# Kernel tuning notes

Hardware: AMD Instinct MI355X
Metric: run time of the kernel (lower is better)

Reference implementation:

```python
import jax, jax.numpy as jnp
import numpy as np

H = 256          # lstm_size
VOCAB = 6        # num_branches + 1
NBR = 5          # num_branches
TEMP = 5.0
OP_TANH = 1.1 / 2.5
BLOCKS, SEQ = 16, 2048


def setup_inputs() -> dict:
    key = jax.random.key(0)
    ks = jax.random.split(key, 12)
    def gw(k, shape, scale=0.05):
        return jax.random.normal(k, shape, dtype=jnp.float32) * scale
    return {
        "arc": jax.random.randint(ks[0], (BLOCKS, SEQ), 0, VOCAB, dtype=jnp.int32),
        "h0": gw(ks[1], (2, 1, H), 0.01),
        "c0": gw(ks[2], (2, 1, H), 0.01),
        "emb": gw(ks[3], (VOCAB, H)),
        "Wih_f": gw(ks[4], (4 * H, H)), "Whh_f": gw(ks[5], (4 * H, H)),
        "bih_f": jnp.zeros(4 * H, jnp.float32), "bhh_f": jnp.zeros(4 * H, jnp.float32),
        "Wih_b": gw(ks[6], (4 * H, H)), "Whh_b": gw(ks[7], (4 * H, H)),
        "bih_b": jnp.zeros(4 * H, jnp.float32), "bhh_b": jnp.zeros(4 * H, jnp.float32),
        "fcW": gw(ks[8], (NBR, 2 * H)), "fcb": jnp.zeros(NBR, jnp.float32),
    }


def _lstm_dir(x, h0, c0, Wih, Whh, bih, bhh):
    # x: [T,H]; one direction of a 1-layer LSTM, PyTorch gate order (i,f,g,o)
    def step(carry, xt):
        h, c = carry
        g = xt @ Wih.T + h @ Whh.T + bih + bhh          # [4H]
        i, f, gg, o = jnp.split(g, 4)
        i, f, o = jax.nn.sigmoid(i), jax.nn.sigmoid(f), jax.nn.sigmoid(o)
        c = f * c + i * jnp.tanh(gg)
        h = o * jnp.tanh(c)
        return (h, c), h
    (hT, cT), hs = jax.lax.scan(step, (h0, c0), x)
    return hs, hT, cT


def reference(arc, h0, c0, emb, Wih_f, Whh_f, bih_f, bhh_f,
              Wih_b, Whh_b, bih_b, bhh_b, fcW, fcb):
    key0 = jax.random.key(42)

    def block(carry, arc_i):
        hf, cf, hb, cb, key = carry
        key, sub = jax.random.split(key)
        x = emb[arc_i]                                   # [T,H]
        hs_f, hfT, cfT = _lstm_dir(x, hf, cf, Wih_f, Whh_f, bih_f, bhh_f)
        hs_b, hbT, cbT = _lstm_dir(x[::-1], hb, cb, Wih_b, Whh_b, bih_b, bhh_b)
        out = jnp.concatenate([hs_f, hs_b[::-1]], axis=-1)   # [T,2H]
        logits = (out @ fcW.T + fcb) / TEMP
        logits = OP_TANH * jnp.tanh(logits)              # [T,5]
        logp = jax.nn.log_softmax(logits, axis=-1)
        prob = jnp.exp(logp)
        idx = jax.random.categorical(sub, logits, axis=-1)   # multinomial(softmax(logits))
        # F.cross_entropy(logits, idx) == mean NLL of sampled indices
        ce = -jnp.mean(jnp.take_along_axis(logp, idx[:, None], axis=-1))
        # original: -mean(sum(logp*prob over size-1 dim)) == -mean over [T,5]
        ent = jax.lax.stop_gradient(-jnp.mean(logp * prob))
        return (hfT, cfT, hbT, cbT, key), (idx, ce, ent)

    init = (h0[0, 0], c0[0, 0], h0[1, 0], c0[1, 0], key0)
    (hfT, cfT, hbT, cbT, _), (all_arc, ces, ents) = jax.lax.scan(block, init, arc)
    h = jnp.stack([hfT, hbT])[:, None, :]                # [2,1,H]
    c = jnp.stack([cfT, cbT])[:, None, :]
    return all_arc, jnp.sum(ces), jnp.sum(ents), h, c
```

## Files before the change

kernel.cpp:

```cpp
#include <hip/hip_runtime.h>
#include <math.h>
#include <stdint.h>

static constexpr int XG_OFF   = 0;
static constexpr int MBA_OFF  = 12288;
static constexpr int MBB_OFF  = 14336;
static constexpr int ELEC_OFF = 16384;
static constexpr int SH_OFF   = 20480;
static constexpr int SC_OFF   = 20992;
static constexpr int HIST_OFF = 21504;
static constexpr int HIST_D   = 524288;
static constexpr int CEP_OFF  = 1070080;
static constexpr int ENTP_OFF = 1070144;

static constexpr int OUT_CE = 32768;
static constexpr int OUT_H  = 32770;
static constexpr int OUT_C  = 33282;

__device__ __forceinline__ void st_sc0(unsigned long long* p, unsigned long long v) {
  asm volatile("global_store_dwordx2 %0, %1, off sc0" :: "v"(p), "v"(v) : "memory");
}
__device__ __forceinline__ unsigned long long ld_sc0(const unsigned long long* p) {
  unsigned long long r;
  asm volatile("global_load_dwordx2 %0, %1, off sc0\n\ts_waitcnt vmcnt(0)"
               : "=&v"(r) : "v"(p) : "memory");
  return r;
}

__device__ __forceinline__ uint32_t rotl32(uint32_t v, int n) {
  return (v << n) | (v >> (32 - n));
}
__device__ __forceinline__ void tf2x32(uint32_t k0, uint32_t k1,
                                       uint32_t x0, uint32_t x1,
                                       uint32_t& y0, uint32_t& y1) {
  const uint32_t k2 = k0 ^ k1 ^ 0x1BD11BDAu;
  x0 += k0; x1 += k1;
  x0 += x1; x1 = rotl32(x1, 13); x1 ^= x0;
  x0 += x1; x1 = rotl32(x1, 15); x1 ^= x0;
  x0 += x1; x1 = rotl32(x1, 26); x1 ^= x0;
  x0 += x1; x1 = rotl32(x1, 6);  x1 ^= x0;
  x0 += k1; x1 += k2 + 1u;
  x0 += x1; x1 = rotl32(x1, 17); x1 ^= x0;
  x0 += x1; x1 = rotl32(x1, 29); x1 ^= x0;
  x0 += x1; x1 = rotl32(x1, 16); x1 ^= x0;
  x0 += x1; x1 = rotl32(x1, 24); x1 ^= x0;
  x0 += k2; x1 += k0 + 2u;
  x0 += x1; x1 = rotl32(x1, 13); x1 ^= x0;
  x0 += x1; x1 = rotl32(x1, 15); x1 ^= x0;
  x0 += x1; x1 = rotl32(x1, 26); x1 ^= x0;
  x0 += x1; x1 = rotl32(x1, 6);  x1 ^= x0;
  x0 += k0; x1 += k1 + 3u;
  x0 += x1; x1 = rotl32(x1, 17); x1 ^= x0;
  x0 += x1; x1 = rotl32(x1, 29); x1 ^= x0;
  x0 += x1; x1 = rotl32(x1, 16); x1 ^= x0;
  x0 += x1; x1 = rotl32(x1, 24); x1 ^= x0;
  x0 += k1; x1 += k2 + 4u;
  x0 += x1; x1 = rotl32(x1, 13); x1 ^= x0;
  x0 += x1; x1 = rotl32(x1, 15); x1 ^= x0;
  x0 += x1; x1 = rotl32(x1, 26); x1 ^= x0;
  x0 += x1; x1 = rotl32(x1, 6);  x1 ^= x0;
  x0 += k2; x1 += k0 + 5u;
  y0 = x0; y1 = x1;
}

__device__ __forceinline__ float gumbel_from_bits(uint32_t bits) {
  float f = __uint_as_float(0x3f800000u | (bits >> 9)) - 1.0f;
  const float tiny = __uint_as_float(0x00800000u);
  float u = fmaxf(tiny, f + tiny);
  float l1 = (float)log((double)u);
  return -(float)log(-(double)l1);
}

__global__ void k_xg(const float* __restrict__ emb,
                     const float* __restrict__ WihF, const float* __restrict__ bihF,
                     const float* __restrict__ bhhF,
                     const float* __restrict__ WihB, const float* __restrict__ bihB,
                     const float* __restrict__ bhhB,
                     float* __restrict__ ws) {
  __shared__ float se[1536];
  const int tid = threadIdx.x;
  for (int i = tid; i < 1536; i += 256) se[i] = emb[i];
  __syncthreads();
  const int gid = blockIdx.x * 256 + tid;
  const int d = gid >> 10, r = gid & 1023;
  const float* Wih = d ? WihB : WihF;
  const float* bih = d ? bihB : bihF;
  const float* bhh = d ? bhhB : bhhF;
  float acc[6] = {0.f, 0.f, 0.f, 0.f, 0.f, 0.f};
  const float4* wr = (const float4*)(Wih + r * 256);
  for (int c = 0; c < 64; c++) {
    float4 wv = wr[c];
#pragma unroll
    for (int v = 0; v < 6; v++) {
      const float* ev = &se[v * 256 + 4 * c];
      acc[v] += wv.x * ev[0] + wv.y * ev[1] + wv.z * ev[2] + wv.w * ev[3];
    }
  }
  const float bsum = bih[r] + bhh[r];
#pragma unroll
  for (int v = 0; v < 6; v++) ws[XG_OFF + d * 6144 + v * 1024 + r] = acc[v] + bsum;
}

__global__ void k_zero(float* __restrict__ ws) {
  if (threadIdx.x < 16) ((int*)(ws + ELEC_OFF))[threadIdx.x] = 0;
}

__global__ __launch_bounds__(256, 1)
void k_chain(const int* __restrict__ arc, const float* __restrict__ h0,
             const float* __restrict__ c0, const float* __restrict__ WhhF,
             const float* __restrict__ WhhB, float* __restrict__ ws,
             float* __restrict__ out, int b) {
  const int tid = threadIdx.x;
  __shared__ int role_s;
  __shared__ float xg_l[768];
  __shared__ int arc_s[2048];
  __shared__ float h_s[2][320];

  if (tid == 0) {
    int xcc;
    asm volatile("s_getreg_b32 %0, hwreg(HW_REG_XCC_ID)" : "=s"(xcc));
    xcc &= 7;
    int* cnt = (int*)(ws + ELEC_OFF);
    int* winner = cnt + 8;
    int pos = __hip_atomic_fetch_add(&cnt[xcc], 1, __ATOMIC_RELAXED,
                                     __HIP_MEMORY_SCOPE_AGENT);
    if (pos == 15) {
      int expected = 0;
      __hip_atomic_compare_exchange_strong(winner, &expected, xcc + 1,
          __ATOMIC_RELAXED, __ATOMIC_RELAXED, __HIP_MEMORY_SCOPE_AGENT);
    }
    int wv;
    do {
      wv = __hip_atomic_load(winner, __ATOMIC_RELAXED, __HIP_MEMORY_SCOPE_AGENT);
    } while (wv == 0);
    role_s = (pos < 16 && wv == xcc + 1) ? pos : -1;
  }
  __syncthreads();
  const int role = role_s;
  if (role < 0) return;

  const int d = role >> 3;
  const int k = role & 7;
  const int w = tid >> 6;
  const int lane = tid & 63;
  const int q = lane >> 4, p = lane & 15;

  const float* Whh = d ? WhhB : WhhF;
  for (int i = tid; i < 768; i += 256) {
    const int sym = i >> 7, r = i & 127, el = r >> 2, g = r & 3;
    xg_l[i] = ws[XG_OFF + d * 6144 + sym * 1024 + g * 256 + 32 * k + el];
  }
  {
    const int* ab = arc + b * 2048;
    for (int i = tid; i < 2048; i += 256) arc_s[i] = ab[i];
  }
  const int eA = 32 * k + 8 * w + 2 * q;
  const int elA = 8 * w + 2 * q;
  float Wr[8][16];
#pragma unroll
  for (int i = 0; i < 8; i++) {
    const int R = 256 * (i >> 1) + eA + (i & 1);
    const float4* rp = (const float4*)(Whh + R * 256 + 16 * p);
#pragma unroll
    for (int j = 0; j < 4; j++) {
      const float4 v = rp[j];
      Wr[i][4 * j + 0] = v.x;
      Wr[i][4 * j + 1] = v.y;
      Wr[i][4 * j + 2] = v.z;
      Wr[i][4 * j + 3] = v.w;
    }
  }
#pragma unroll
  for (int i = 0; i < 8; i++)
#pragma unroll
    for (int c = 0; c < 16; c++)
      asm volatile("" : "+v"(Wr[i][c]));
  const float* hprev = (b == 0) ? (h0 + d * 256) : (ws + SH_OFF + d * 256);
  float4 hw[4];
#pragma unroll
  for (int j = 0; j < 4; j++) hw[j] = ((const float4*)(hprev + 16 * p))[j];
  float cA = (b == 0) ? c0[d * 256 + eA] : ws[SC_OFF + d * 256 + eA];
  float cB = (b == 0) ? c0[d * 256 + eA + 1] : ws[SC_OFF + d * 256 + eA + 1];
  float hA = 0.f, hB = 0.f;
  __syncthreads();

  unsigned long long* mbA = (unsigned long long*)(ws + MBA_OFF);
  unsigned long long* mbB = (unsigned long long*)(ws + MBB_OFF);
  const unsigned stampBase = (unsigned)b * 2048u;
  float* histD = ws + HIST_OFF + d * HIST_D;
  const bool selfPoll = ((tid >> 5) == k);
  int lim = 24, fails = 0;

  for (int t = 0; t < 2048; t++) {
    float acc[8];
#pragma unroll
    for (int i = 0; i < 8; i++) {
      float a;
      a  = Wr[i][0]  * hw[0].x;
      a += Wr[i][1]  * hw[0].y;
      a += Wr[i][2]  * hw[0].z;
      a += Wr[i][3]  * hw[0].w;
      a += Wr[i][4]  * hw[1].x;
      a += Wr[i][5]  * hw[1].y;
      a += Wr[i][6]  * hw[1].z;
      a += Wr[i][7]  * hw[1].w;
      a += Wr[i][8]  * hw[2].x;
      a += Wr[i][9]  * hw[2].y;
      a += Wr[i][10] * hw[2].z;
      a += Wr[i][11] * hw[2].w;
      a += Wr[i][12] * hw[3].x;
      a += Wr[i][13] * hw[3].y;
      a += Wr[i][14] * hw[3].z;
      a += Wr[i][15] * hw[3].w;
      acc[i] = a;
    }
#pragma unroll
    for (int i = 0; i < 8; i++) {
      float v = acc[i];
      v += __shfl_xor(v, 1, 16);
      v += __shfl_xor(v, 2, 16);
      v += __shfl_xor(v, 4, 16);
      v += __shfl_xor(v, 8, 16);
      acc[i] = v;
    }
    const int sym = arc_s[d ? (2047 - t) : t];
    const float4 xgA = *(const float4*)&xg_l[sym * 128 + elA * 4];
    const float4 xgB = *(const float4*)&xg_l[sym * 128 + elA * 4 + 4];
    {
      const float gi = acc[0] + xgA.x;
      const float gf = acc[2] + xgA.y;
      const float gg = acc[4] + xgA.z;
      const float go = acc[6] + xgA.w;
      const float I = 1.0f / (1.0f + expf(-gi));
      const float F = 1.0f / (1.0f + expf(-gf));
      const float G = tanhf(gg);
      const float O = 1.0f / (1.0f + expf(-go));
      cA = F * cA + I * G;
      hA = O * tanhf(cA);
    }
    {
      const float gi = acc[1] + xgB.x;
      const float gf = acc[3] + xgB.y;
      const float gg = acc[5] + xgB.z;
      const float go = acc[7] + xgB.w;
      const float I = 1.0f / (1.0f + expf(-gi));
      const float F = 1.0f / (1.0f + expf(-gf));
      const float G = tanhf(gg);
      const float O = 1.0f / (1.0f + expf(-go));
      cB = F * cB + I * G;
      hB = O * tanhf(cB);
    }
    const unsigned S = stampBase + (unsigned)t + 1u;
    const int mbo = (d * 2 + (t & 1)) * 256;
    unsigned long long* mbAp = mbA + mbo;
    unsigned long long* mbBp = mbB + mbo;
    const int np = (t + 1) & 1;
    if (p < 2) {
      const int e = eA + p;
      const float hv = p ? hB : hA;
      const unsigned long long pk = (unsigned long long)__float_as_uint(hv) |
                                    ((unsigned long long)S << 32);
      __hip_atomic_store(&mbBp[e], pk, __ATOMIC_RELAXED, __HIP_MEMORY_SCOPE_AGENT);
      st_sc0(&mbAp[e], pk);
      histD[t * 256 + e] = hv;
      h_s[np][(e >> 4) * 20 + (e & 15)] = hv;
    }
    asm volatile("s_waitcnt vmcnt(0)" ::: "memory");
    if (t == 2047) break;
    {
      unsigned long long v = 0;
      bool got = false;
      for (int it = 0; it < lim; ++it) {
        unsigned long long f = selfPoll ? 0ull : ld_sc0(&mbAp[tid]);
        bool ok = selfPoll | ((unsigned)(f >> 32) == S);
        if (__all(ok)) { v = f; got = true; break; }
      }
      if (!got) {
        if (++fails >= 4) lim = 0;
        for (;;) {
          unsigned long long f = selfPoll ? 0ull :
              __hip_atomic_load(&mbBp[tid], __ATOMIC_RELAXED,
                                __HIP_MEMORY_SCOPE_AGENT);
          bool ok = selfPoll | ((unsigned)(f >> 32) == S);
          if (__all(ok)) { v = f; break; }
        }
      }
      if (!selfPoll)
        h_s[np][(tid >> 4) * 20 + (tid & 15)] = __uint_as_float((unsigned)v);
    }
    __syncthreads();
    {
      const float4* hp = (const float4*)&h_s[np][20 * p];
#pragma unroll
      for (int j = 0; j < 4; j++) hw[j] = hp[j];
    }
  }

  if (p < 2) {
    const int e = eA + p;
    ws[SH_OFF + d * 256 + e] = p ? hB : hA;
    ws[SC_OFF + d * 256 + e] = p ? cB : cA;
    if (b == 15) {
      out[OUT_H + d * 256 + e] = p ? hB : hA;
      out[OUT_C + d * 256 + e] = p ? cB : cA;
    }
  }
}

__global__ void k_sampler(const float* __restrict__ fcW, const float* __restrict__ fcb,
                          float* __restrict__ ws, float* __restrict__ out, int b) {
  const int tid = threadIdx.x;
  __shared__ float sW[5 * 512];
  __shared__ float sb[5];
  __shared__ float red[256];
  for (int i = tid; i < 2560; i += 256) sW[i] = fcW[i];
  if (tid < 5) sb[tid] = fcb[tid];
  __syncthreads();
  uint32_t s0 = 0u, s1 = 0u;
  {
    uint32_t k0 = 0u, k1 = 42u;
    for (int i = 0; i <= b; i++) {
      uint32_t n0, n1, t0, t1;
      tf2x32(k0, k1, 0u, 0u, n0, n1);
      tf2x32(k0, k1, 0u, 1u, t0, t1);
      s0 = t0; s1 = t1;
      k0 = n0; k1 = n1;
    }
  }
  const int pp = blockIdx.x * 256 + tid;
  const float* histF = ws + HIST_OFF;
  const float* histB = ws + HIST_OFF + HIST_D;
  float dotL[5] = {0.f, 0.f, 0.f, 0.f, 0.f};
  float dotH[5] = {0.f, 0.f, 0.f, 0.f, 0.f};
  const float4* hfL = (const float4*)(histF + pp * 256);
  const float4* hbL = (const float4*)(histB + (2047 - pp) * 256);
  const float4* hfH = (const float4*)(histF + (pp + 1024) * 256);
  const float4* hbH = (const float4*)(histB + (1023 - pp) * 256);
  for (int c = 0; c < 64; c++) {
    float4 a = hfL[c], bb = hbL[c], e = hfH[c], f = hbH[c];
#pragma unroll
    for (int j = 0; j < 5; j++) {
      const float* wr = &sW[j * 512 + 4 * c];
      dotL[j] += a.x * wr[0] + a.y * wr[1] + a.z * wr[2] + a.w * wr[3];
      dotL[j] += bb.x * wr[256] + bb.y * wr[257] + bb.z * wr[258] + bb.w * wr[259];
      dotH[j] += e.x * wr[0] + e.y * wr[1] + e.z * wr[2] + e.w * wr[3];
      dotH[j] += f.x * wr[256] + f.y * wr[257] + f.z * wr[258] + f.w * wr[259];
    }
  }
  uint32_t bl[5], bh[5];
#pragma unroll
  for (int j = 0; j < 5; j++) {
    uint32_t y0, y1;
    tf2x32(s0, s1, 0u, (uint32_t)(5 * pp + j), y0, y1);
    bl[j] = y0 ^ y1;
    tf2x32(s0, s1, 0u, (uint32_t)(5 * (pp + 1024) + j), y0, y1);
    bh[j] = y0 ^ y1;
  }
  const float OPT = (float)(1.1 / 2.5);
  float ce_acc = 0.f, ent_acc = 0.f;
#pragma unroll
  for (int half = 0; half < 2; half++) {
    const int t = half ? (pp + 1024) : pp;
    float l[5];
#pragma unroll
    for (int j = 0; j < 5; j++) {
      float dv = half ? dotH[j] : dotL[j];
      l[j] = OPT * tanhf((dv + sb[j]) / 5.0f);
    }
    int idx = 0;
    float best;
    {
      uint32_t b0 = half ? bh[0] : bl[0];
      best = gumbel_from_bits(b0) + l[0];
    }
#pragma unroll
    for (int j = 1; j < 5; j++) {
      uint32_t bj = half ? bh[j] : bl[j];
      float v = gumbel_from_bits(bj) + l[j];
      if (v > best) { best = v; idx = j; }
    }
    out[b * 2048 + t] = (float)idx;
    float m = l[0];
#pragma unroll
    for (int j = 1; j < 5; j++) m = fmaxf(m, l[j]);
    float ssum = 0.f;
#pragma unroll
    for (int j = 0; j < 5; j++) ssum += expf(l[j] - m);
    float lse = logf(ssum);
    float lpidx = 0.f;
#pragma unroll
    for (int j = 0; j < 5; j++) {
      float lp = (l[j] - m) - lse;
      ent_acc -= lp * expf(lp);
      lpidx = (j == idx) ? lp : lpidx;
    }
    ce_acc -= lpidx;
  }
  red[tid] = ce_acc; __syncthreads();
  for (int s = 128; s > 0; s >>= 1) {
    if (tid < s) red[tid] += red[tid + s];
    __syncthreads();
  }
  if (tid == 0) ws[CEP_OFF + b * 4 + blockIdx.x] = red[0];
  __syncthreads();
  red[tid] = ent_acc; __syncthreads();
  for (int s = 128; s > 0; s >>= 1) {
    if (tid < s) red[tid] += red[tid + s];
    __syncthreads();
  }
  if (tid == 0) ws[ENTP_OFF + b * 4 + blockIdx.x] = red[0];
}

__global__ void k_final(const float* __restrict__ ws, float* __restrict__ out) {
  if (threadIdx.x == 0 && blockIdx.x == 0) {
    float ce = 0.f, ent = 0.f;
    for (int b = 0; b < 16; b++) {
      float cb = 0.f, eb = 0.f;
      for (int j = 0; j < 4; j++) {
        cb += ws[CEP_OFF + b * 4 + j];
        eb += ws[ENTP_OFF + b * 4 + j];
      }
      ce += cb / 2048.0f;
      ent += eb / 10240.0f;
    }
    out[OUT_CE] = ce;
    out[OUT_CE + 1] = ent;
  }
}

extern "C" void kernel_launch(void* const* d_in, const int* in_sizes, int n_in,
                              void* d_out, int out_size, void* d_ws, size_t ws_size,
                              hipStream_t stream) {
  (void)in_sizes; (void)n_in; (void)out_size; (void)ws_size;
  const int* arc = (const int*)d_in[0];
  const float* h0 = (const float*)d_in[1];
  const float* c0 = (const float*)d_in[2];
  const float* emb = (const float*)d_in[3];
  const float* WihF = (const float*)d_in[4];
  const float* WhhF = (const float*)d_in[5];
  const float* bihF = (const float*)d_in[6];
  const float* bhhF = (const float*)d_in[7];
  const float* WihB = (const float*)d_in[8];
  const float* WhhB = (const float*)d_in[9];
  const float* bihB = (const float*)d_in[10];
  const float* bhhB = (const float*)d_in[11];
  const float* fcW = (const float*)d_in[12];
  const float* fcb = (const float*)d_in[13];
  float* out = (float*)d_out;
  float* ws = (float*)d_ws;

  hipLaunchKernelGGL(k_xg, dim3(8), dim3(256), 0, stream,
                     emb, WihF, bihF, bhhF, WihB, bihB, bhhB, ws);
  for (int b = 0; b < 16; b++) {
    hipLaunchKernelGGL(k_zero, dim3(1), dim3(64), 0, stream, ws);
    hipLaunchKernelGGL(k_chain, dim3(128), dim3(256), 0, stream,
                       arc, h0, c0, WhhF, WhhB, ws, out, b);
    hipLaunchKernelGGL(k_sampler, dim3(4), dim3(256), 0, stream,
                       fcW, fcb, ws, out, b);
  }
  hipLaunchKernelGGL(k_final, dim3(1), dim3(64), 0, stream, ws, out);
}
```

Before: 63.25 ms.

## Spread mailbox polling across non-producer lanes and keep losing blocks spinning

Each non-producer lane now polls one remote mailbox entry with per-lane retry loops, replacing the wave-wide __all polling over 256 entries with self-skip. The vmcnt(0) wait after stores is removed, and the full __syncthreads becomes lgkmcnt wait plus a raw s_barrier. Blocks that lose the election no longer exit. They spin on FMA work until role 0 sets a done flag, apparently to keep clocks or occupancy steady. The risks are memory-ordering hazards from dropping the vmcnt wait, and wasted power from the spinning blocks.

Result: slower. 68.72 ms (+8.6%).

```diff
diff --git a/kernel.cpp b/kernel.cpp
--- a/kernel.cpp
+++ b/kernel.cpp
@@ -137,7 +137,18 @@
   }
   __syncthreads();
   const int role = role_s;
-  if (role < 0) return;
+  if (role < 0) {
+    int* done = (int*)(ws + ELEC_OFF) + 9;
+    float x = (float)tid + 1.5f;
+    for (;;) {
+#pragma unroll
+      for (int i = 0; i < 512; i++) x = __builtin_fmaf(x, 1.0000001f, 1e-7f);
+      asm volatile("" : "+v"(x));
+      if (__hip_atomic_load(done, __ATOMIC_RELAXED, __HIP_MEMORY_SCOPE_AGENT) != 0)
+        break;
+    }
+    return;
+  }
 
   const int d = role >> 3;
   const int k = role & 7;
@@ -188,7 +199,12 @@
   unsigned long long* mbB = (unsigned long long*)(ws + MBB_OFF);
   const unsigned stampBase = (unsigned)b * 2048u;
   float* histD = ws + HIST_OFF + d * HIST_D;
-  const bool selfPoll = ((tid >> 5) == k);
+  const bool producer = (p < 2);
+  int pollE = -1;
+  if (p >= 2) {
+    const int pi = (4 * w + q) * 14 + (p - 2);
+    pollE = pi + (pi >= 32 * k ? 32 : 0);
+  }
   int lim = 24, fails = 0;
 
   for (int t = 0; t < 2048; t++) {
@@ -255,7 +271,7 @@
     unsigned long long* mbAp = mbA + mbo;
     unsigned long long* mbBp = mbB + mbo;
     const int np = (t + 1) & 1;
-    if (p < 2) {
+    if (producer) {
       const int e = eA + p;
       const float hv = p ? hB : hA;
       const unsigned long long pk = (unsigned long long)__float_as_uint(hv) |
@@ -265,30 +281,26 @@
       histD[t * 256 + e] = hv;
       h_s[np][(e >> 4) * 20 + (e & 15)] = hv;
     }
-    asm volatile("s_waitcnt vmcnt(0)" ::: "memory");
     if (t == 2047) break;
-    {
+    if (pollE >= 0) {
       unsigned long long v = 0;
       bool got = false;
       for (int it = 0; it < lim; ++it) {
-        unsigned long long f = selfPoll ? 0ull : ld_sc0(&mbAp[tid]);
-        bool ok = selfPoll | ((unsigned)(f >> 32) == S);
-        if (__all(ok)) { v = f; got = true; break; }
+        unsigned long long f = ld_sc0(&mbAp[pollE]);
+        if ((unsigned)(f >> 32) == S) { v = f; got = true; break; }
       }
       if (!got) {
         if (++fails >= 4) lim = 0;
-        for (;;) {
-          unsigned long long f = selfPoll ? 0ull :
-              __hip_atomic_load(&mbBp[tid], __ATOMIC_RELAXED,
+        do {
+          v = __hip_atomic_load(&mbBp[pollE], __ATOMIC_RELAXED,
                                 __HIP_MEMORY_SCOPE_AGENT);
-          bool ok = selfPoll | ((unsigned)(f >> 32) == S);
-          if (__all(ok)) { v = f; break; }
-        }
+        } while ((unsigned)(v >> 32) != S);
       }
-      if (!selfPoll)
-        h_s[np][(tid >> 4) * 20 + (tid & 15)] = __uint_as_float((unsigned)v);
-    }
-    __syncthreads();
+      h_s[np][(pollE >> 4) * 20 + (pollE & 15)] = __uint_as_float((unsigned)v);
+    }
+    asm volatile("s_waitcnt lgkmcnt(0)" ::: "memory");
+    __builtin_amdgcn_s_barrier();
+    __builtin_amdgcn_sched_barrier(0);
     {
       const float4* hp = (const float4*)&h_s[np][20 * p];
 #pragma unroll
@@ -296,7 +308,7 @@
     }
   }
 
-  if (p < 2) {
+  if (producer) {
     const int e = eA + p;
     ws[SH_OFF + d * 256 + e] = p ? hB : hA;
     ws[SC_OFF + d * 256 + e] = p ? cB : cA;
@@ -305,6 +317,9 @@
       out[OUT_C + d * 256 + e] = p ? cB : cA;
     }
   }
+  if (role == 0 && tid == 0)
+    __hip_atomic_store(((int*)(ws + ELEC_OFF)) + 9, 1, __ATOMIC_RELAXED,
+                       __HIP_MEMORY_SCOPE_AGENT);
 }
 
 __global__ void k_sampler(const float* __restrict__ fcW, const float* __restrict__ fcb,
```
